# Kernel optimization log

Measured on AMD Instinct MI355X. Metric: run time of the kernel, lower is better.

Reference implementation:

```python
import jax, jax.numpy as jnp
import numpy as np
from jax import lax

# dims
BS, C, H, W = 16, 684, 32, 128   # batch, encoder channels, feature-map H/W
Q, K, PAD = 256, 11, 5           # coverage channels, conv_Q kernel, padding
N, NP = 256, 512                 # decoder hidden n, attention dim n_prime
T = 4                            # prior attention steps stored in alpha


def setup_inputs() -> dict:
    key = jax.random.key(0)
    ks = jax.random.split(key, 10)
    s = 0.02  # small init scale (stand-in for xavier)
    return {
        "x": jax.random.normal(ks[0], (BS, C, H, W), jnp.float32),
        "st_hat": jax.random.normal(ks[1], (BS, 1, N), jnp.float32),
        "alpha": jax.random.uniform(ks[2], (BS, T, H * W), jnp.float32),
        # conv_Q: Conv2d(1, Q, k=11, pad=5)
        "convQ_w": jax.random.normal(ks[3], (Q, 1, K, K), jnp.float32) * s,
        "convQ_b": jnp.zeros((Q,), jnp.float32),
        # fc_Wa: Linear(n, n_prime)
        "Wa_w": jax.random.normal(ks[4], (NP, N), jnp.float32) * s,
        "Wa_b": jnp.zeros((NP,), jnp.float32),
        # conv_Ua: Conv2d(C, n_prime, k=1)
        "convUa_w": jax.random.normal(ks[5], (NP, C, 1, 1), jnp.float32) * s,
        "convUa_b": jnp.zeros((NP,), jnp.float32),
        # fc_Uf: Linear(Q, n_prime)
        "Uf_w": jax.random.normal(ks[6], (NP, Q), jnp.float32) * s,
        "Uf_b": jnp.zeros((NP,), jnp.float32),
        # fc_Va: Linear(n_prime, 1)
        "Va_w": jax.random.normal(ks[7], (1, NP), jnp.float32) * s,
        "Va_b": jnp.zeros((1,), jnp.float32),
    }


def reference(x, st_hat, alpha, convQ_w, convQ_b, Wa_w, Wa_b,
              convUa_w, convUa_b, Uf_w, Uf_b, Va_w, Va_b):
    bs, c, h, w = x.shape
    # beta: sum of past attention maps -> [bs, 1, h, w]
    beta = alpha.sum(axis=1).reshape(bs, 1, h, w)
    # conv_Q: coverage features [bs, Q, h, w]
    Fc = lax.conv_general_dilated(
        beta, convQ_w, window_strides=(1, 1), padding=[(PAD, PAD), (PAD, PAD)],
        dimension_numbers=("NCHW", "OIHW", "NCHW")) + convQ_b[None, :, None, None]
    # fc_Uf over channel dim after permute(2,3,0,1): [h, w, bs, n_prime]
    cover = jnp.einsum("bqhw,pq->hwbp", Fc, Uf_w) + Uf_b
    # conv_Ua (1x1 conv == per-pixel linear): [h, w, bs, n_prime]
    key = jnp.einsum("bchw,pc->hwbp", x, convUa_w[:, :, 0, 0]) + convUa_b
    # fc_Wa(st_hat).squeeze(1): [bs, n_prime]
    query = st_hat[:, 0, :] @ Wa_w.T + Wa_b
    # additive attention score
    score = jnp.tanh(key + query[None, None, :, :] + cover)  # [h,w,bs,np]
    # fc_Va -> e_t, permuted to [bs, h*w] (row-major over h,w like torch view)
    e = jnp.einsum("hwbp,p->bhw", score, Va_w[0]) + Va_b[0]
    e = e.reshape(bs, h * w)
    # softmax with the module's explicit exp/sum + eps formulation
    e_exp = jnp.exp(e)
    alpha_t = e_exp / (e_exp.sum(axis=1, keepdims=True) + 1e-8)  # [bs, hw]
    # context vector g_t = sum_n alpha_t[b,n] * x[b,c,n]
    context = jnp.einsum("bn,bcn->bc", alpha_t, x.reshape(bs, c, h * w))
    return context, alpha_t.reshape(bs, 1, h, w)
```

## Files before the change

### kernel.cpp

```cpp
#include <hip/hip_runtime.h>
#include <math.h>

#define BS 16
#define C_ 684
#define Hh 32
#define Ww 128
#define HW 4096
#define Qc 256
#define NP 512
#define Nn 256
#define NKT 26
#define NB 64

#define WS_BETA 0
#define WS_BIAS 65536
#define WS_EEXP 73728
#define WS_INV  139264
#define WS_ASW  139280

typedef __attribute__((ext_vector_type(8))) short bf16x8;
typedef __attribute__((ext_vector_type(4))) float f32x4;

static __device__ __forceinline__ short f2bf(float f) {
    unsigned u = __builtin_bit_cast(unsigned, f);
    u += 0x7fff + ((u >> 16) & 1);
    return (short)(u >> 16);
}

static __device__ __forceinline__ float fast_tanh(float v) {
    float ax = fabsf(v);
    float t = __expf(-2.f * ax);
    float th = (1.f - t) * __builtin_amdgcn_rcpf(1.f + t);
    return copysignf(th, v);
}

__global__ void k_prep(const float* __restrict__ alpha, const float* __restrict__ ua,
                       const float* __restrict__ ufw, const float* __restrict__ qw,
                       const float* __restrict__ st, const float* __restrict__ waw,
                       const float* __restrict__ wab, const float* __restrict__ ufb,
                       const float* __restrict__ qb, const float* __restrict__ uab,
                       float* __restrict__ beta, short* __restrict__ a_sw,
                       float* __restrict__ bias) {
    int part = blockIdx.x, tid = threadIdx.x;
    if (part < 256) {
        int idx = part * 256 + tid;
        int b = idx >> 12, n = idx & 4095;
        const float* a = alpha + (size_t)b * 4 * HW + n;
        beta[idx] = a[0] + a[HW] + a[2 * HW] + a[3 * HW];
    } else if (part < 1920) {
        int idx = (part - 256) * 256 + tid;
        int j = idx & 7, m = (idx >> 3) & 511, g = (idx >> 12) & 3, kt = idx >> 14;
        int k = kt * 32 + g * 8 + j;
        float v = 0.f;
        if (k < C_) {
            v = ua[m * C_ + k];
        } else if (k < C_ + 121) {
            int tap = k - C_;
            const float* ur = ufw + m * Qc;
            float s = 0.f;
            for (int q = 0; q < Qc; ++q) s += ur[q] * qw[q * 121 + tap];
            v = s;
        }
        a_sw[idx] = f2bf(v);
    } else {
        int idx = (part - 1920) * 256 + tid;
        int b = idx >> 9, p = idx & 511;
        float s = wab[p] + ufb[p] + uab[p];
        const float* sv = st + b * Nn;
        const float* wr = waw + p * Nn;
        for (int n = 0; n < Nn; ++n) s += sv[n] * wr[n];
        const float* ur = ufw + p * Qc;
        for (int q = 0; q < Qc; ++q) s += ur[q] * qb[q];
        bias[idx] = s;
    }
}

__launch_bounds__(256, 2)
__global__ void k_gemm(const short* __restrict__ a_sw, const float* __restrict__ x,
                       const float* __restrict__ beta, const float* __restrict__ bias,
                       const float* __restrict__ vaw, const float* __restrict__ vab,
                       float* __restrict__ eexp) {
    __shared__ short Bs[4 * NB * 8];
    __shared__ float ered[4][NB];

    const int tid = threadIdx.x;
    const int lane = tid & 63, wid = tid >> 6;
    const int b = blockIdx.y, n0 = blockIdx.x * NB;
    const int q = lane >> 4, r = lane & 15;

    const int sn = tid & 63;
    const int sg = tid >> 6;
    const int n_glob = n0 + sn;
    const int pr = n_glob >> 7, pc = n_glob & 127;
    const float* xb = x + (size_t)b * C_ * HW + n_glob;
    const float* betab = beta + b * HW;

    f32x4 acc[8][4] = {};

    for (int kt = 0; kt < NKT; ++kt) {
        const short* ag = a_sw + kt * (4 * NP * 8);
        bf16x8 af[8];
        #pragma unroll
        for (int ms = 0; ms < 8; ++ms)
            af[ms] = *(const bf16x8*)(ag + (size_t)(q * NP + wid * 128 + ms * 16 + r) * 8);

        unsigned pk[4];
        {
            int kbase = kt * 32 + sg * 8;
            #pragma unroll
            for (int half = 0; half < 4; ++half) {
                unsigned w = 0;
                #pragma unroll
                for (int t = 0; t < 2; ++t) {
                    int k = kbase + half * 2 + t;
                    float f = 0.f;
                    if (k < C_) {
                        f = xb[(size_t)k * HW];
                    } else if (k < C_ + 121) {
                        int tap = k - C_;
                        int di = tap / 11, dj = tap - di * 11;
                        int rr = pr + di - 5, cc = pc + dj - 5;
                        if (rr >= 0 && rr < Hh && cc >= 0 && cc < Ww)
                            f = betab[rr * 128 + cc];
                    }
                    w |= ((unsigned)(unsigned short)f2bf(f)) << (16 * t);
                }
                pk[half] = w;
            }
        }
        __syncthreads();
        *(uint4*)&Bs[(sg * NB + sn) * 8] = make_uint4(pk[0], pk[1], pk[2], pk[3]);
        __syncthreads();

        bf16x8 bf[4];
        #pragma unroll
        for (int ns = 0; ns < 4; ++ns)
            bf[ns] = *(const bf16x8*)&Bs[(q * NB + ns * 16 + r) * 8];
        #pragma unroll
        for (int ms = 0; ms < 8; ++ms)
            #pragma unroll
            for (int ns = 0; ns < 4; ++ns)
                acc[ms][ns] = __builtin_amdgcn_mfma_f32_16x16x32_bf16(af[ms], bf[ns], acc[ms][ns], 0, 0, 0);
    }

    float es[4] = {0.f, 0.f, 0.f, 0.f};
    #pragma unroll
    for (int ms = 0; ms < 8; ++ms) {
        #pragma unroll
        for (int reg = 0; reg < 4; ++reg) {
            int row = wid * 128 + ms * 16 + q * 4 + reg;
            float bv = bias[b * NP + row];
            float vv = vaw[row];
            #pragma unroll
            for (int ns = 0; ns < 4; ++ns)
                es[ns] += vv * fast_tanh(acc[ms][ns][reg] + bv);
        }
    }
    #pragma unroll
    for (int ns = 0; ns < 4; ++ns) {
        es[ns] += __shfl_xor(es[ns], 16, 64);
        es[ns] += __shfl_xor(es[ns], 32, 64);
    }
    if (lane < 16) {
        #pragma unroll
        for (int ns = 0; ns < 4; ++ns) ered[wid][ns * 16 + r] = es[ns];
    }
    __syncthreads();
    if (tid < NB) {
        float s = ered[0][tid] + ered[1][tid] + ered[2][tid] + ered[3][tid] + vab[0];
        eexp[b * HW + n0 + tid] = expf(s);
    }
}

__global__ void k_sum(const float* __restrict__ eexp, float* __restrict__ inv) {
    __shared__ float sred[256];
    int b = blockIdx.x, tid = threadIdx.x;
    const float4* er = (const float4*)(eexp + b * HW);
    float ps = 0.f;
    for (int k = tid; k < 1024; k += 256) {
        float4 v = er[k];
        ps += v.x + v.y + v.z + v.w;
    }
    sred[tid] = ps;
    __syncthreads();
    for (int s = 128; s > 0; s >>= 1) {
        if (tid < s) sred[tid] += sred[tid + s];
        __syncthreads();
    }
    if (tid == 0) inv[b] = 1.f / (sred[0] + 1e-8f);
}

__global__ void k_finish(const float* __restrict__ x, const float* __restrict__ eexp,
                         const float* __restrict__ inv, float* __restrict__ ctx,
                         float* __restrict__ aout) {
    __shared__ float sred[256];
    int c = blockIdx.x, b = blockIdx.y, tid = threadIdx.x;
    float iv = inv[b];
    if (c == C_) {
        for (int k = tid; k < HW; k += 256) aout[b * HW + k] = eexp[b * HW + k] * iv;
        return;
    }
    const float4* xr = (const float4*)(x + ((size_t)b * C_ + c) * HW);
    const float4* er = (const float4*)(eexp + b * HW);
    float acc = 0.f;
    for (int k = tid; k < 1024; k += 256) {
        float4 xv = xr[k], ev = er[k];
        acc += xv.x * ev.x + xv.y * ev.y + xv.z * ev.z + xv.w * ev.w;
    }
    sred[tid] = acc;
    __syncthreads();
    for (int s = 128; s > 0; s >>= 1) {
        if (tid < s) sred[tid] += sred[tid + s];
        __syncthreads();
    }
    if (tid == 0) ctx[b * C_ + c] = sred[0] * iv;
}

extern "C" void kernel_launch(void* const* d_in, const int* in_sizes, int n_in,
                              void* d_out, int out_size, void* d_ws, size_t ws_size,
                              hipStream_t stream) {
    const float* x      = (const float*)d_in[0];
    const float* st     = (const float*)d_in[1];
    const float* alpha  = (const float*)d_in[2];
    const float* convQw = (const float*)d_in[3];
    const float* convQb = (const float*)d_in[4];
    const float* Waw    = (const float*)d_in[5];
    const float* Wab    = (const float*)d_in[6];
    const float* Uaw    = (const float*)d_in[7];
    const float* Uab    = (const float*)d_in[8];
    const float* Ufw    = (const float*)d_in[9];
    const float* Ufb    = (const float*)d_in[10];
    const float* Vaw    = (const float*)d_in[11];
    const float* Vab    = (const float*)d_in[12];

    float* ws   = (float*)d_ws;
    float* beta = ws + WS_BETA;
    float* bias = ws + WS_BIAS;
    float* eexp = ws + WS_EEXP;
    float* inv  = ws + WS_INV;
    short* a_sw = (short*)(ws + WS_ASW);

    float* ctx  = (float*)d_out;
    float* aout = (float*)d_out + BS * C_;

    k_prep<<<1952, 256, 0, stream>>>(alpha, Uaw, Ufw, convQw, st, Waw, Wab, Ufb,
                                     convQb, Uab, beta, a_sw, bias);
    k_gemm<<<dim3(HW / NB, BS), 256, 0, stream>>>(a_sw, x, beta, bias, Vaw, Vab, eexp);
    k_sum<<<BS, 256, 0, stream>>>(eexp, inv);
    k_finish<<<dim3(C_ + 1, BS), 256, 0, stream>>>(x, eexp, inv, ctx, aout);
}
```

Baseline: 429.7 us.

## Prefetch GEMM B operand two stages ahead, fuse softmax sum via atomics, warp-per-channel finish

The GEMM kernel now loads the x/beta operand for stage kt+2 into registers while the current stage's MFMAs run, and issues the A-fragment loads after the LDS barrier, so global-load latency can hide behind compute. The separate softmax-sum kernel is removed: each GEMM block reduces its exp values with a wavefront shuffle and atomically adds them into a per-batch sum that k_prep zeroes. The finish kernel assigns one wavefront per channel instead of one block, using shuffle reductions in place of LDS tree reductions. The trade-offs are extra register pressure from the prefetch buffers and atomic float accumulation whose ordering is nondeterministic.

```diff
diff --git a/kernel.cpp b/kernel.cpp
--- a/kernel.cpp
+++ b/kernel.cpp
@@ -15,7 +15,7 @@
 #define WS_BETA 0
 #define WS_BIAS 65536
 #define WS_EEXP 73728
-#define WS_INV  139264
+#define WS_ESUM 139264
 #define WS_ASW  139280
 
 typedef __attribute__((ext_vector_type(8))) short bf16x8;
@@ -40,7 +40,7 @@
                        const float* __restrict__ wab, const float* __restrict__ ufb,
                        const float* __restrict__ qb, const float* __restrict__ uab,
                        float* __restrict__ beta, short* __restrict__ a_sw,
-                       float* __restrict__ bias) {
+                       float* __restrict__ bias, float* __restrict__ esum) {
     int part = blockIdx.x, tid = threadIdx.x;
     if (part < 256) {
         int idx = part * 256 + tid;
@@ -62,7 +62,7 @@
             v = s;
         }
         a_sw[idx] = f2bf(v);
-    } else {
+    } else if (part < 1952) {
         int idx = (part - 1920) * 256 + tid;
         int b = idx >> 9, p = idx & 511;
         float s = wab[p] + ufb[p] + uab[p];
@@ -72,6 +72,8 @@
         const float* ur = ufw + p * Qc;
         for (int q = 0; q < Qc; ++q) s += ur[q] * qb[q];
         bias[idx] = s;
+    } else {
+        if (tid < BS) esum[tid] = 0.f;
     }
 }
 
@@ -79,7 +81,7 @@
 __global__ void k_gemm(const short* __restrict__ a_sw, const float* __restrict__ x,
                        const float* __restrict__ beta, const float* __restrict__ bias,
                        const float* __restrict__ vaw, const float* __restrict__ vab,
-                       float* __restrict__ eexp) {
+                       float* __restrict__ eexp, float* __restrict__ esum) {
     __shared__ short Bs[4 * NB * 8];
     __shared__ float ered[4][NB];
 
@@ -96,52 +98,67 @@
     const float* betab = beta + b * HW;
 
     f32x4 acc[8][4] = {};
-
+    float fv[2][8];
+
+    #define LDSTAGE(KT, DST)                                                  \
+    {                                                                         \
+        int kbase = (KT) * 32 + sg * 8;                                       \
+        _Pragma("unroll")                                                     \
+        for (int j = 0; j < 8; ++j) {                                         \
+            int k = kbase + j;                                                \
+            float f = 0.f;                                                    \
+            if (k < C_) {                                                     \
+                f = xb[(size_t)k * HW];                                       \
+            } else if (k < C_ + 121) {                                        \
+                int tap = k - C_;                                             \
+                int di = tap / 11, dj = tap - di * 11;                        \
+                int rr = pr + di - 5, cc = pc + dj - 5;                       \
+                if (rr >= 0 && rr < Hh && cc >= 0 && cc < Ww)                 \
+                    f = betab[rr * 128 + cc];                                 \
+            }                                                                 \
+            (DST)[j] = f;                                                     \
+        }                                                                     \
+    }
+
+    LDSTAGE(0, fv[0]);
+    LDSTAGE(1, fv[1]);
+
+    const short* ap = a_sw + (size_t)(q * NP + wid * 128 + r) * 8;
+
+    #pragma unroll 2
     for (int kt = 0; kt < NKT; ++kt) {
-        const short* ag = a_sw + kt * (4 * NP * 8);
-        bf16x8 af[8];
-        #pragma unroll
-        for (int ms = 0; ms < 8; ++ms)
-            af[ms] = *(const bf16x8*)(ag + (size_t)(q * NP + wid * 128 + ms * 16 + r) * 8);
-
-        unsigned pk[4];
+        __syncthreads();
         {
-            int kbase = kt * 32 + sg * 8;
+            const float* f = fv[kt & 1];
+            unsigned pk[4];
             #pragma unroll
-            for (int half = 0; half < 4; ++half) {
-                unsigned w = 0;
-                #pragma unroll
-                for (int t = 0; t < 2; ++t) {
-                    int k = kbase + half * 2 + t;
-                    float f = 0.f;
-                    if (k < C_) {
-                        f = xb[(size_t)k * HW];
-                    } else if (k < C_ + 121) {
-                        int tap = k - C_;
-                        int di = tap / 11, dj = tap - di * 11;
-                        int rr = pr + di - 5, cc = pc + dj - 5;
-                        if (rr >= 0 && rr < Hh && cc >= 0 && cc < Ww)
-                            f = betab[rr * 128 + cc];
-                    }
-                    w |= ((unsigned)(unsigned short)f2bf(f)) << (16 * t);
-                }
-                pk[half] = w;
-            }
+            for (int h = 0; h < 4; ++h)
+                pk[h] = (unsigned)(unsigned short)f2bf(f[2 * h]) |
+                        ((unsigned)(unsigned short)f2bf(f[2 * h + 1]) << 16);
+            *(uint4*)&Bs[(sg * NB + sn) * 8] = make_uint4(pk[0], pk[1], pk[2], pk[3]);
         }
         __syncthreads();
-        *(uint4*)&Bs[(sg * NB + sn) * 8] = make_uint4(pk[0], pk[1], pk[2], pk[3]);
-        __syncthreads();
 
         bf16x8 bf[4];
         #pragma unroll
         for (int ns = 0; ns < 4; ++ns)
             bf[ns] = *(const bf16x8*)&Bs[(q * NB + ns * 16 + r) * 8];
+
+        bf16x8 af[8];
+        const short* ak = ap + (size_t)kt * 4 * NP * 8;
+        #pragma unroll
+        for (int ms = 0; ms < 8; ++ms)
+            af[ms] = *(const bf16x8*)(ak + ms * 16 * 8);
+
+        if (kt < NKT - 2) LDSTAGE(kt + 2, fv[kt & 1]);
+
         #pragma unroll
         for (int ms = 0; ms < 8; ++ms)
             #pragma unroll
             for (int ns = 0; ns < 4; ++ns)
                 acc[ms][ns] = __builtin_amdgcn_mfma_f32_16x16x32_bf16(af[ms], bf[ns], acc[ms][ns], 0, 0, 0);
     }
+    #undef LDSTAGE
 
     float es[4] = {0.f, 0.f, 0.f, 0.f};
     #pragma unroll
@@ -168,52 +185,37 @@
     __syncthreads();
     if (tid < NB) {
         float s = ered[0][tid] + ered[1][tid] + ered[2][tid] + ered[3][tid] + vab[0];
-        eexp[b * HW + n0 + tid] = expf(s);
-    }
-}
-
-__global__ void k_sum(const float* __restrict__ eexp, float* __restrict__ inv) {
-    __shared__ float sred[256];
-    int b = blockIdx.x, tid = threadIdx.x;
-    const float4* er = (const float4*)(eexp + b * HW);
-    float ps = 0.f;
-    for (int k = tid; k < 1024; k += 256) {
-        float4 v = er[k];
-        ps += v.x + v.y + v.z + v.w;
-    }
-    sred[tid] = ps;
-    __syncthreads();
-    for (int s = 128; s > 0; s >>= 1) {
-        if (tid < s) sred[tid] += sred[tid + s];
-        __syncthreads();
-    }
-    if (tid == 0) inv[b] = 1.f / (sred[0] + 1e-8f);
+        float ex = expf(s);
+        eexp[b * HW + n0 + tid] = ex;
+        float ps = ex;
+        #pragma unroll
+        for (int off = 32; off > 0; off >>= 1) ps += __shfl_xor(ps, off, 64);
+        if (tid == 0) atomicAdd(&esum[b], ps);
+    }
 }
 
 __global__ void k_finish(const float* __restrict__ x, const float* __restrict__ eexp,
-                         const float* __restrict__ inv, float* __restrict__ ctx,
+                         const float* __restrict__ esum, float* __restrict__ ctx,
                          float* __restrict__ aout) {
-    __shared__ float sred[256];
-    int c = blockIdx.x, b = blockIdx.y, tid = threadIdx.x;
-    float iv = inv[b];
-    if (c == C_) {
+    int part = blockIdx.x, b = blockIdx.y, tid = threadIdx.x;
+    float iv = 1.f / (esum[b] + 1e-8f);
+    if (part == 171) {
         for (int k = tid; k < HW; k += 256) aout[b * HW + k] = eexp[b * HW + k] * iv;
         return;
     }
+    int wid = tid >> 6, lane = tid & 63;
+    int c = part * 4 + wid;
     const float4* xr = (const float4*)(x + ((size_t)b * C_ + c) * HW);
     const float4* er = (const float4*)(eexp + b * HW);
     float acc = 0.f;
-    for (int k = tid; k < 1024; k += 256) {
+    #pragma unroll 4
+    for (int k = lane; k < 1024; k += 64) {
         float4 xv = xr[k], ev = er[k];
         acc += xv.x * ev.x + xv.y * ev.y + xv.z * ev.z + xv.w * ev.w;
     }
-    sred[tid] = acc;
-    __syncthreads();
-    for (int s = 128; s > 0; s >>= 1) {
-        if (tid < s) sred[tid] += sred[tid + s];
-        __syncthreads();
-    }
-    if (tid == 0) ctx[b * C_ + c] = sred[0] * iv;
+    #pragma unroll
+    for (int off = 32; off > 0; off >>= 1) acc += __shfl_xor(acc, off, 64);
+    if (lane == 0) ctx[b * C_ + c] = acc * iv;
 }
 
 extern "C" void kernel_launch(void* const* d_in, const int* in_sizes, int n_in,
@@ -237,15 +239,14 @@
     float* beta = ws + WS_BETA;
     float* bias = ws + WS_BIAS;
     float* eexp = ws + WS_EEXP;
-    float* inv  = ws + WS_INV;
+    float* esum = ws + WS_ESUM;
     short* a_sw = (short*)(ws + WS_ASW);
 
     float* ctx  = (float*)d_out;
     float* aout = (float*)d_out + BS * C_;
 
-    k_prep<<<1952, 256, 0, stream>>>(alpha, Uaw, Ufw, convQw, st, Waw, Wab, Ufb,
-                                     convQb, Uab, beta, a_sw, bias);
-    k_gemm<<<dim3(HW / NB, BS), 256, 0, stream>>>(a_sw, x, beta, bias, Vaw, Vab, eexp);
-    k_sum<<<BS, 256, 0, stream>>>(eexp, inv);
-    k_finish<<<dim3(C_ + 1, BS), 256, 0, stream>>>(x, eexp, inv, ctx, aout);
-}
+    k_prep<<<1953, 256, 0, stream>>>(alpha, Uaw, Ufw, convQw, st, Waw, Wab, Ufb,
+                                     convQb, Uab, beta, a_sw, bias, esum);
+    k_gemm<<<dim3(HW / NB, BS), 256, 0, stream>>>(a_sw, x, beta, bias, Vaw, Vab, eexp, esum);
+    k_finish<<<dim3(172, BS), 256, 0, stream>>>(x, eexp, esum, ctx, aout);
+}
```

Result: faster. 369.5 us (-14.0%).
